# Kernel optimization log

Measured on AMD Instinct MI355X. Metric: run time of the kernel, lower is better.

## Reference

```python
import jax, jax.numpy as jnp
import numpy as np

N_WORDS, MAX_LEN, EMB, HID, VOCAB = 100000, 24, 50, 50, 200


def setup_inputs() -> dict:
    key = jax.random.key(0)
    ks = jax.random.split(key, 9)
    s = 0.1
    char_indices = jax.random.randint(ks[0], (N_WORDS, MAX_LEN), 0, VOCAB, dtype=jnp.int32)
    lengths = jax.random.randint(ks[1], (N_WORDS,), 0, MAX_LEN + 1, dtype=jnp.int32)
    emb_table = (jax.random.normal(ks[2], (VOCAB, EMB), jnp.float32) * s).at[0].set(0.0)  # padding_idx=0
    Wih_f = jax.random.normal(ks[3], (4 * HID, EMB), jnp.float32) * s
    Whh_f = jax.random.normal(ks[4], (4 * HID, HID), jnp.float32) * s
    b_f = jax.random.normal(ks[5], (4 * HID,), jnp.float32) * s  # b_ih + b_hh combined
    Wih_b = jax.random.normal(ks[6], (4 * HID, EMB), jnp.float32) * s
    Whh_b = jax.random.normal(ks[7], (4 * HID, HID), jnp.float32) * s
    b_b = jax.random.normal(ks[8], (4 * HID,), jnp.float32) * s
    return {"char_indices": char_indices, "lengths": lengths, "emb_table": emb_table,
            "Wih_f": Wih_f, "Whh_f": Whh_f, "b_f": b_f,
            "Wih_b": Wih_b, "Whh_b": Whh_b, "b_b": b_b}


def _lstm_final(emb_seq, mask_seq, Wih, Whh, b):
    # emb_seq: [T, N, E], mask_seq: [T, N] (True while t < length)
    # Masked updates freeze (h, c) past each word's length, so the final carry
    # equals PyTorch's h_n for that direction.
    hdim = Whh.shape[1]
    n = emb_seq.shape[1]

    def step(carry, xs):
        h, c = carry
        x, m = xs
        g = x @ Wih.T + h @ Whh.T + b  # [N, 4H], gate order i,f,g,o (PyTorch)
        i, f, gg, o = jnp.split(g, 4, axis=-1)
        c_new = jax.nn.sigmoid(f) * c + jax.nn.sigmoid(i) * jnp.tanh(gg)
        h_new = jax.nn.sigmoid(o) * jnp.tanh(c_new)
        m = m[:, None]
        return (jnp.where(m, h_new, h), jnp.where(m, c_new, c)), None

    h0 = jnp.zeros((n, hdim), emb_seq.dtype)
    (h_fin, _), _ = jax.lax.scan(step, (h0, h0), (emb_seq, mask_seq))
    return h_fin


def reference(char_indices, lengths, emb_table, Wih_f, Whh_f, b_f, Wih_b, Whh_b, b_b):
    n, t_max = char_indices.shape
    t = jnp.arange(t_max)
    mask = t[None, :] < lengths[:, None]  # [N, T]
    emb = emb_table[char_indices]  # [N, T, E]
    h_fwd = _lstm_final(emb.transpose(1, 0, 2), mask.T, Wih_f, Whh_f, b_f)
    # Backward direction: reverse valid prefix of each word, then scan forward.
    rev_pos = jnp.clip(lengths[:, None] - 1 - t[None, :], 0, t_max - 1)  # [N, T]
    emb_rev = emb_table[jnp.take_along_axis(char_indices, rev_pos, axis=1)]
    h_bwd = _lstm_final(emb_rev.transpose(1, 0, 2), mask.T, Wih_b, Whh_b, b_b)
    return jnp.concatenate([h_fwd, h_bwd], axis=-1)  # [N, 2H]
```

## Files before the change

kernel.cpp:

```cpp
#include <hip/hip_runtime.h>

#define EMBD 50
#define HID 50
#define BLK 256
#define NT 13
#define LOG2E 1.44269504f

typedef float f32x4 __attribute__((ext_vector_type(4)));
typedef short short8 __attribute__((ext_vector_type(8)));
typedef unsigned u32x4 __attribute__((ext_vector_type(4)));

__device__ __forceinline__ int imax(int a, int b) { return a > b ? a : b; }
__device__ __forceinline__ int imin(int a, int b) { return a < b ? a : b; }

__device__ __forceinline__ unsigned short f2bf(float f) {
    unsigned u = __float_as_uint(f);
    u += 0x7FFFu + ((u >> 16) & 1u);
    return (unsigned short)(u >> 16);
}
__device__ __forceinline__ unsigned cvtpk(float a, float b) {
    unsigned r;
    asm("v_cvt_pk_bf16_f32 %0, %1, %2" : "=v"(r) : "v"(a), "v"(b));
    return r;
}
__device__ __forceinline__ float sigm(float x) {
    return __fdividef(1.0f, 1.0f + __expf(-x));
}
__device__ __forceinline__ float tanhfast(float x) {
    float e = __expf(2.0f * x);
    return 1.0f - __fdividef(2.0f, e + 1.0f);
}

__global__ void zero_counts_kernel(int* ws) {
    if (threadIdx.x < 75) ws[threadIdx.x] = 0;
}
__global__ void hist_kernel(const int* __restrict__ lengths, int* ws, int nw) {
    __shared__ int lc[32];
    if (threadIdx.x < 32) lc[threadIdx.x] = 0;
    __syncthreads();
    int i = blockIdx.x * blockDim.x + threadIdx.x;
    if (i < nw) atomicAdd(&lc[lengths[i]], 1);
    __syncthreads();
    if (threadIdx.x < 25 && lc[threadIdx.x] > 0)
        atomicAdd(&ws[threadIdx.x], lc[threadIdx.x]);
}
__global__ void prefix_kernel(int* ws) {
    if (threadIdx.x == 0 && blockIdx.x == 0) {
        int acc = 0;
        for (int l = 0; l <= 24; ++l) { ws[25 + l] = acc; acc += ws[l]; }
    }
}
__global__ void scatter_kernel(const int* __restrict__ lengths, int* ws, int nw) {
    __shared__ int lcnt[32], lbase[32];
    if (threadIdx.x < 32) lcnt[threadIdx.x] = 0;
    __syncthreads();
    int i = blockIdx.x * blockDim.x + threadIdx.x;
    int l = 0, ticket = 0;
    bool act = i < nw;
    if (act) {
        l = lengths[i];
        ticket = atomicAdd(&lcnt[l], 1);
    }
    __syncthreads();
    if (threadIdx.x < 25 && lcnt[threadIdx.x] > 0)
        lbase[threadIdx.x] = atomicAdd(&ws[50 + threadIdx.x], lcnt[threadIdx.x]);
    __syncthreads();
    if (act) ws[100 + ws[25 + l] + lbase[l] + ticket] = i;
}

__global__ void pack_all_kernel(const float* __restrict__ emb,
                                const float* __restrict__ Wih_f, const float* __restrict__ Whh_f,
                                const float* __restrict__ b_f,
                                const float* __restrict__ Wih_b, const float* __restrict__ Whh_b,
                                const float* __restrict__ b_b,
                                unsigned short* __restrict__ xtab,
                                unsigned short* __restrict__ wp, int vocab) {
    int tid0 = blockIdx.x * blockDim.x + threadIdx.x;
    int xtTotal = 2 * vocab * NT * 16;
    if (tid0 < xtTotal) {
        int q = tid0 & 3, s = (tid0 >> 2) & 3;
        int m = (tid0 >> 4) % NT;
        int vv = (tid0 >> 4) / NT;
        int v = vv % vocab, dir = vv / vocab;
        int cnt_s = (s < 2) ? 13 : 12;
        float val = 0.0f;
        if (m < cnt_s) {
            int j = 13 * s - (s == 3 ? 1 : 0) + m;
            int row = q * HID + j;
            const float* W  = dir ? Wih_b : Wih_f;
            const float* bv = dir ? b_b   : b_f;
            float acc = bv[row];
            const float* wr = W + row * EMBD;
            const float* ev = emb + v * EMBD;
            for (int e = 0; e < EMBD; ++e) acc += wr[e] * ev[e];
            val = acc * ((q == 2) ? (2.0f * LOG2E) : LOG2E);
        }
        xtab[tid0] = f2bf(val);
        return;
    }
    int tid = tid0 - xtTotal;
    if (tid >= 2 * NT * 1024) return;
    int i    = tid & 7;
    int lane = (tid >> 3) & 63;
    int kcp  = (tid >> 9) & 1;
    int rem  = tid >> 10;
    int m    = rem % NT;
    int dir  = rem / NT;
    const float* Whh = dir ? Whh_b : Whh_f;

    int p = lane & 15, grp = lane >> 4;
    int k = (kcp + 2) * 32 + 8 * grp + i;
    int s = p >> 2, q = p & 3;
    int cnt_s = (s < 2) ? 13 : 12;
    float val = 0.0f;
    if (m < cnt_s) {
        int j = 13 * s - (s == 3 ? 1 : 0) + m;
        int row = q * HID + j;
        int kk = k - 64;
        int half = kk >> 5;
        int s2 = (kk >> 3) & 3;
        int r = kk & 7;
        int mcol = half * 8 + r;
        int cnt2 = (s2 < 2) ? 13 : 12;
        if (mcol < cnt2) {
            int jc = 13 * s2 - (s2 == 3 ? 1 : 0) + mcol;
            val = Whh[row * HID + jc] * ((q == 2) ? (2.0f * LOG2E) : LOG2E);
        }
    }
    wp[tid] = f2bf(val);
}

#define MFMA16(AW, BB, ACC) __builtin_amdgcn_mfma_f32_16x16x32_bf16((AW), (BB), (ACC), 0, 0, 0)

#define TTMH(M, XT, C, H) {                                        \
    const short8 w2 = *(const short8*)(sWl + ((M)*2+0)*512);       \
    const short8 w3 = *(const short8*)(sWl + ((M)*2+1)*512);       \
    f32x4 ah = zz;                                                 \
    ah = MFMA16(w2, bh0, ah);                                      \
    ah = MFMA16(w3, bh1, ah);                                      \
    float ai = ah[0] + __uint_as_float((XT).x << 16);              \
    float af = ah[1] + __uint_as_float((XT).x & 0xffff0000u);      \
    float ag = ah[2] + __uint_as_float((XT).y << 16);              \
    float ao = ah[3] + __uint_as_float((XT).y & 0xffff0000u);      \
    float ei = __builtin_amdgcn_exp2f(-ai);                        \
    float ef = __builtin_amdgcn_exp2f(-af);                        \
    float eg = __builtin_amdgcn_exp2f(ag);                         \
    float eo = __builtin_amdgcn_exp2f(-ao);                        \
    float a1 = 1.0f + ef, a2 = 1.0f + ei;                          \
    float a3 = eg + 1.0f, a4 = eg - 1.0f;                          \
    float p1 = a2 * a3;                                            \
    float nn = fmaf(a1, a4, (C) * p1);                             \
    float dd = a1 * p1;                                            \
    float cn = nn * __builtin_amdgcn_rcpf(dd);                     \
    float ec = __builtin_amdgcn_exp2f((2.0f * LOG2E) * cn);        \
    float b2 = ec + 1.0f, b3 = ec - 1.0f;                          \
    float qd = (1.0f + eo) * b2;                                   \
    float hn = b3 * __builtin_amdgcn_rcpf(qd);                     \
    (C) = upd ? cn : (C);                                          \
    (H) = upd ? hn : (H); }

__global__ __launch_bounds__(BLK, 2)
void bilstm_mfma_kernel(const int* __restrict__ chars,
                        const int* __restrict__ lengths,
                        const int* __restrict__ perm,
                        const unsigned short* __restrict__ xtab,
                        const unsigned short* __restrict__ wp,
                        float* __restrict__ out, int nw, int ml, int vocab)
{
    const int dir = blockIdx.y;
    __shared__ unsigned short sW[NT * 2 * 512];
    {
        const float4* src = (const float4*)(wp + dir * (NT * 2 * 512));
        float4* dst = (float4*)sW;
        for (int i = threadIdx.x; i < NT * 2 * 512 / 8; i += BLK) dst[i] = src[i];
    }
    __syncthreads();

    const int lane = threadIdx.x & 63;
    const int wv   = threadIdx.x >> 6;
    const int wcol = lane & 15;
    const int s    = lane >> 4;

    int gidx = (blockIdx.x * 4 + wv) * 16 + wcol;
    gidx = imin(gidx, nw - 1);
    gidx = nw - 1 - gidx;
    const int word = perm[gidx];
    const int len  = lengths[word];

    int lmax = len;
    lmax = imax(lmax, __shfl_xor(lmax, 1));
    lmax = imax(lmax, __shfl_xor(lmax, 2));
    lmax = imax(lmax, __shfl_xor(lmax, 4));
    lmax = imax(lmax, __shfl_xor(lmax, 8));

    const int* charp = chars + (size_t)word * ml;
    const unsigned short* sWl = sW + lane * 8;
    const unsigned short* xdir = xtab + (size_t)dir * vocab * (NT * 16) + s * 4;

    const f32x4 zz = {0.0f, 0.0f, 0.0f, 0.0f};
    float c00=0,c01=0,c02=0,c03=0,c04=0,c05=0,c06=0,c07=0,c08=0,c09=0,c10=0,c11=0,c12=0;
    float h00=0,h01=0,h02=0,h03=0,h04=0,h05=0,h06=0,h07=0,h08=0,h09=0,h10=0,h11=0,h12=0;
    short8 bh0, bh1;
#pragma unroll
    for (int i2 = 0; i2 < 8; ++i2) { bh0[i2] = 0; bh1[i2] = 0; }

    int chcur = 0;
    if (lmax > 0) {
        int pos0 = dir ? imax(len - 1, 0) : 0;
        chcur = charp[pos0];
    }

    for (int t = 0; t < lmax; ++t) {
        const unsigned short* xb = xdir + (size_t)chcur * (NT * 16);
        uint2 xt0  = *(const uint2*)(xb + 0*16);
        uint2 xt1  = *(const uint2*)(xb + 1*16);
        uint2 xt2  = *(const uint2*)(xb + 2*16);
        uint2 xt3  = *(const uint2*)(xb + 3*16);
        uint2 xt4  = *(const uint2*)(xb + 4*16);
        uint2 xt5  = *(const uint2*)(xb + 5*16);
        uint2 xt6  = *(const uint2*)(xb + 6*16);
        uint2 xt7  = *(const uint2*)(xb + 7*16);
        uint2 xt8  = *(const uint2*)(xb + 8*16);
        uint2 xt9  = *(const uint2*)(xb + 9*16);
        uint2 xt10 = *(const uint2*)(xb + 10*16);
        uint2 xt11 = *(const uint2*)(xb + 11*16);
        uint2 xt12 = *(const uint2*)(xb + 12*16);

        int tn = (t + 1 < lmax) ? t + 1 : t;
        int posn = dir ? imax(len - 1 - tn, 0) : tn;
        int chnext = charp[posn];

        const bool upd = (t < len);
        TTMH(0,  xt0,  c00, h00)
        TTMH(1,  xt1,  c01, h01)
        TTMH(2,  xt2,  c02, h02)
        TTMH(3,  xt3,  c03, h03)
        TTMH(4,  xt4,  c04, h04)
        TTMH(5,  xt5,  c05, h05)
        TTMH(6,  xt6,  c06, h06)
        TTMH(7,  xt7,  c07, h07)
        TTMH(8,  xt8,  c08, h08)
        TTMH(9,  xt9,  c09, h09)
        TTMH(10, xt10, c10, h10)
        TTMH(11, xt11, c11, h11)
        TTMH(12, xt12, c12, h12)

        u32x4 p0, p1;
        p0[0] = cvtpk(h00, h01); p0[1] = cvtpk(h02, h03);
        p0[2] = cvtpk(h04, h05); p0[3] = cvtpk(h06, h07);
        p1[0] = cvtpk(h08, h09); p1[1] = cvtpk(h10, h11);
        p1[2] = cvtpk(h12, 0.0f); p1[3] = 0u;
        bh0 = __builtin_bit_cast(short8, p0);
        bh1 = __builtin_bit_cast(short8, p1);

        chcur = chnext;
    }

    int offs = 13 * s - (s == 3 ? 1 : 0);
    float* outw = out + (size_t)word * (2 * HID) + dir * HID + offs;
    outw[0] = h00; outw[1] = h01; outw[2]  = h02; outw[3]  = h03;
    outw[4] = h04; outw[5] = h05; outw[6]  = h06; outw[7]  = h07;
    outw[8] = h08; outw[9] = h09; outw[10] = h10; outw[11] = h11;
    if (s < 2) outw[12] = h12;
}

__global__ __launch_bounds__(BLK, 2)
void bilstm_fallback_kernel(const int* __restrict__ chars,
                            const int* __restrict__ lengths,
                            const float* __restrict__ emb,
                            const float* __restrict__ Wih_f, const float* __restrict__ Whh_f, const float* __restrict__ b_f,
                            const float* __restrict__ Wih_b, const float* __restrict__ Whh_b, const float* __restrict__ b_b,
                            const int* __restrict__ perm,
                            float* __restrict__ out, int nw, int ml)
{
    const int dir = blockIdx.y;
    const float* Wih = dir ? Wih_b : Wih_f;
    const float* Whh = dir ? Whh_b : Whh_f;
    const float* bv  = dir ? b_b  : b_f;
    __shared__ float4 sWU4[HID * 100];
    __shared__ float4 sB4[HID];
    {
        float* p = (float*)sWU4;
        for (int i = threadIdx.x; i < HID * 100 * 4; i += BLK) {
            int g = i & 3, r = i >> 2, j = r / 100, k = r - j * 100;
            p[i] = (k < EMBD) ? Wih[(j + g * HID) * EMBD + k]
                              : Whh[(j + g * HID) * HID + (k - EMBD)];
        }
        if (threadIdx.x < HID) {
            int j = threadIdx.x;
            sB4[j] = make_float4(bv[j], bv[j + HID], bv[j + 2*HID], bv[j + 3*HID]);
        }
    }
    __syncthreads();
    int gid = blockIdx.x * BLK + threadIdx.x;
    if (gid >= nw) return;
    int word = perm ? perm[gid] : gid;
    int len  = lengths[word];
    float h[HID], x[EMBD], c[HID], hn[HID];
#pragma unroll
    for (int j = 0; j < HID; ++j) h[j] = 0.f;
#pragma unroll 1
    for (int j = 0; j < HID; ++j) c[j] = 0.f;
    const int* wch = chars + word * ml;
    float* op = out + (size_t)word * (2 * HID) + dir * HID;
#pragma unroll 1
    for (int t = 0; t < len; ++t) {
        int pos = dir ? (len - 1 - t) : t;
        int ch = wch[pos];
        const float2* ep = (const float2*)(emb + ch * EMBD);
#pragma unroll
        for (int k = 0; k < EMBD / 2; ++k) { float2 v = ep[k]; x[2*k] = v.x; x[2*k+1] = v.y; }
#pragma unroll 1
        for (int j = 0; j < HID; ++j) {
            const float4* wpt = sWU4 + j * 100;
            float4 bb = sB4[j];
            float gi = bb.x, gf = bb.y, gg = bb.z, go = bb.w;
#pragma unroll
            for (int k = 0; k < EMBD; ++k) {
                float4 w = wpt[k]; float xv = x[k];
                gi += w.x*xv; gf += w.y*xv; gg += w.z*xv; go += w.w*xv;
            }
#pragma unroll
            for (int k = 0; k < HID; ++k) {
                float4 w = wpt[EMBD + k]; float hv = h[k];
                gi += w.x*hv; gf += w.y*hv; gg += w.z*hv; go += w.w*hv;
            }
            float cn = sigm(gf) * c[j] + sigm(gi) * tanhfast(gg);
            c[j] = cn;
            hn[j] = sigm(go) * tanhfast(cn);
        }
#pragma unroll
        for (int j = 0; j < HID; ++j) h[j] = hn[j];
    }
#pragma unroll
    for (int j = 0; j < HID / 2; ++j)
        ((float2*)op)[j] = make_float2(h[2*j], h[2*j+1]);
}

extern "C" void kernel_launch(void* const* d_in, const int* in_sizes, int n_in,
                              void* d_out, int out_size, void* d_ws, size_t ws_size,
                              hipStream_t stream) {
    const int*   chars = (const int*)  d_in[0];
    const int*   lens  = (const int*)  d_in[1];
    const float* emb   = (const float*)d_in[2];
    const float* Wih_f = (const float*)d_in[3];
    const float* Whh_f = (const float*)d_in[4];
    const float* b_f   = (const float*)d_in[5];
    const float* Wih_b = (const float*)d_in[6];
    const float* Whh_b = (const float*)d_in[7];
    const float* b_b   = (const float*)d_in[8];
    float* out = (float*)d_out;

    const int nw    = in_sizes[1];
    const int ml    = in_sizes[0] / nw;
    const int vocab = in_sizes[2] / EMBD;

    size_t sortNeed = (size_t)(100 + nw) * 4;
    size_t xtOff    = (sortNeed + 255) & ~(size_t)255;
    size_t xtBytes  = (size_t)2 * vocab * NT * 16 * 2;
    size_t wOff     = (xtOff + xtBytes + 1023) & ~(size_t)1023;
    size_t wBytes   = (size_t)2 * NT * 1024 * 2;
    size_t need     = wOff + wBytes;

    int* ws = (int*)d_ws;
    bool haveSort = ws_size >= sortNeed;
    if (haveSort) {
        zero_counts_kernel<<<1, 128, 0, stream>>>(ws);
        hist_kernel<<<(nw + 255) / 256, 256, 0, stream>>>(lens, ws, nw);
        prefix_kernel<<<1, 1, 0, stream>>>(ws);
        scatter_kernel<<<(nw + 255) / 256, 256, 0, stream>>>(lens, ws, nw);
    }

    if (ws_size >= need && haveSort) {
        unsigned short* xtab = (unsigned short*)((char*)d_ws + xtOff);
        unsigned short* wpk  = (unsigned short*)((char*)d_ws + wOff);
        int packTot = 2 * vocab * NT * 16 + 2 * NT * 1024;
        pack_all_kernel<<<(packTot + 255) / 256, 256, 0, stream>>>(
            emb, Wih_f, Whh_f, b_f, Wih_b, Whh_b, b_b, xtab, wpk, vocab);
        dim3 grid((nw + 63) / 64, 2);
        bilstm_mfma_kernel<<<grid, BLK, 0, stream>>>(chars, lens, ws + 100, xtab, wpk,
                                                     out, nw, ml, vocab);
    } else {
        dim3 grid((nw + BLK - 1) / BLK, 2);
        bilstm_fallback_kernel<<<grid, BLK, 0, stream>>>(chars, lens, emb,
                                                         Wih_f, Whh_f, b_f,
                                                         Wih_b, Whh_b, b_b,
                                                         haveSort ? ws + 100 : nullptr,
                                                         out, nw, ml);
    }
}
```

Measured before the change: 218.4 us.

## Process two independent word groups per wavefront to interleave MFMA chains

Each wavefront now runs two independent batches of 16 words (A and B) in the same time loop. The MFMAs and gate math of the two batches are interleaved, so independent work can hide MFMA and transcendental latency in the serial recurrence, and each shared-memory weight load is reused for both batches. The grid is halved to match and launch bounds drop to one block per SIMD-pair hint, which raises register use and may reduce occupancy. Forward character positions are now clamped to the word length.

```diff
diff --git a/kernel.cpp b/kernel.cpp
--- a/kernel.cpp
+++ b/kernel.cpp
@@ -132,16 +132,11 @@
 
 #define MFMA16(AW, BB, ACC) __builtin_amdgcn_mfma_f32_16x16x32_bf16((AW), (BB), (ACC), 0, 0, 0)
 
-#define TTMH(M, XT, C, H) {                                        \
-    const short8 w2 = *(const short8*)(sWl + ((M)*2+0)*512);       \
-    const short8 w3 = *(const short8*)(sWl + ((M)*2+1)*512);       \
-    f32x4 ah = zz;                                                 \
-    ah = MFMA16(w2, bh0, ah);                                      \
-    ah = MFMA16(w3, bh1, ah);                                      \
-    float ai = ah[0] + __uint_as_float((XT).x << 16);              \
-    float af = ah[1] + __uint_as_float((XT).x & 0xffff0000u);      \
-    float ag = ah[2] + __uint_as_float((XT).y << 16);              \
-    float ao = ah[3] + __uint_as_float((XT).y & 0xffff0000u);      \
+#define GUP(AH, XT, C, H, UPD) {                                   \
+    float ai = (AH)[0] + __uint_as_float((XT).x << 16);            \
+    float af = (AH)[1] + __uint_as_float((XT).x & 0xffff0000u);    \
+    float ag = (AH)[2] + __uint_as_float((XT).y << 16);            \
+    float ao = (AH)[3] + __uint_as_float((XT).y & 0xffff0000u);    \
     float ei = __builtin_amdgcn_exp2f(-ai);                        \
     float ef = __builtin_amdgcn_exp2f(-af);                        \
     float eg = __builtin_amdgcn_exp2f(ag);                         \
@@ -156,10 +151,19 @@
     float b2 = ec + 1.0f, b3 = ec - 1.0f;                          \
     float qd = (1.0f + eo) * b2;                                   \
     float hn = b3 * __builtin_amdgcn_rcpf(qd);                     \
-    (C) = upd ? cn : (C);                                          \
-    (H) = upd ? hn : (H); }
-
-__global__ __launch_bounds__(BLK, 2)
+    (C) = (UPD) ? cn : (C);                                        \
+    (H) = (UPD) ? hn : (H); }
+
+#define TTMH2(M, XTA, XTB, CA, HA, CB, HB) {                       \
+    const short8 w2 = *(const short8*)(sWl + ((M)*2+0)*512);       \
+    const short8 w3 = *(const short8*)(sWl + ((M)*2+1)*512);       \
+    f32x4 ahA = zz, ahB = zz;                                      \
+    ahA = MFMA16(w2, bhA0, ahA);  ahB = MFMA16(w2, bhB0, ahB);     \
+    ahA = MFMA16(w3, bhA1, ahA);  ahB = MFMA16(w3, bhB1, ahB);     \
+    GUP(ahA, XTA, CA, HA, updA)                                    \
+    GUP(ahB, XTB, CB, HB, updB) }
+
+__global__ __launch_bounds__(BLK, 1)
 void bilstm_mfma_kernel(const int* __restrict__ chars,
                         const int* __restrict__ lengths,
                         const int* __restrict__ perm,
@@ -181,87 +185,111 @@
     const int wcol = lane & 15;
     const int s    = lane >> 4;
 
-    int gidx = (blockIdx.x * 4 + wv) * 16 + wcol;
-    gidx = imin(gidx, nw - 1);
-    gidx = nw - 1 - gidx;
-    const int word = perm[gidx];
-    const int len  = lengths[word];
-
-    int lmax = len;
+    int base = (blockIdx.x * 4 + wv) * 32;
+    int giA = imin(base + wcol, nw - 1);
+    int giB = imin(base + 16 + wcol, nw - 1);
+    giA = nw - 1 - giA;
+    giB = nw - 1 - giB;
+    const int wordA = perm[giA];
+    const int wordB = perm[giB];
+    const int lenA  = lengths[wordA];
+    const int lenB  = lengths[wordB];
+
+    int lmax = imax(lenA, lenB);
     lmax = imax(lmax, __shfl_xor(lmax, 1));
     lmax = imax(lmax, __shfl_xor(lmax, 2));
     lmax = imax(lmax, __shfl_xor(lmax, 4));
     lmax = imax(lmax, __shfl_xor(lmax, 8));
 
-    const int* charp = chars + (size_t)word * ml;
+    const int* charpA = chars + (size_t)wordA * ml;
+    const int* charpB = chars + (size_t)wordB * ml;
     const unsigned short* sWl = sW + lane * 8;
     const unsigned short* xdir = xtab + (size_t)dir * vocab * (NT * 16) + s * 4;
 
     const f32x4 zz = {0.0f, 0.0f, 0.0f, 0.0f};
-    float c00=0,c01=0,c02=0,c03=0,c04=0,c05=0,c06=0,c07=0,c08=0,c09=0,c10=0,c11=0,c12=0;
-    float h00=0,h01=0,h02=0,h03=0,h04=0,h05=0,h06=0,h07=0,h08=0,h09=0,h10=0,h11=0,h12=0;
-    short8 bh0, bh1;
-#pragma unroll
-    for (int i2 = 0; i2 < 8; ++i2) { bh0[i2] = 0; bh1[i2] = 0; }
-
-    int chcur = 0;
+    float cA00=0,cA01=0,cA02=0,cA03=0,cA04=0,cA05=0,cA06=0,cA07=0,cA08=0,cA09=0,cA10=0,cA11=0,cA12=0;
+    float hA00=0,hA01=0,hA02=0,hA03=0,hA04=0,hA05=0,hA06=0,hA07=0,hA08=0,hA09=0,hA10=0,hA11=0,hA12=0;
+    float cB00=0,cB01=0,cB02=0,cB03=0,cB04=0,cB05=0,cB06=0,cB07=0,cB08=0,cB09=0,cB10=0,cB11=0,cB12=0;
+    float hB00=0,hB01=0,hB02=0,hB03=0,hB04=0,hB05=0,hB06=0,hB07=0,hB08=0,hB09=0,hB10=0,hB11=0,hB12=0;
+    short8 bhA0, bhA1, bhB0, bhB1;
+#pragma unroll
+    for (int i2 = 0; i2 < 8; ++i2) { bhA0[i2]=0; bhA1[i2]=0; bhB0[i2]=0; bhB1[i2]=0; }
+
+    int chA = 0, chB = 0;
     if (lmax > 0) {
-        int pos0 = dir ? imax(len - 1, 0) : 0;
-        chcur = charp[pos0];
+        int pA = dir ? imax(lenA - 1, 0) : 0;
+        int pB = dir ? imax(lenB - 1, 0) : 0;
+        chA = charpA[pA];
+        chB = charpB[pB];
     }
 
     for (int t = 0; t < lmax; ++t) {
-        const unsigned short* xb = xdir + (size_t)chcur * (NT * 16);
-        uint2 xt0  = *(const uint2*)(xb + 0*16);
-        uint2 xt1  = *(const uint2*)(xb + 1*16);
-        uint2 xt2  = *(const uint2*)(xb + 2*16);
-        uint2 xt3  = *(const uint2*)(xb + 3*16);
-        uint2 xt4  = *(const uint2*)(xb + 4*16);
-        uint2 xt5  = *(const uint2*)(xb + 5*16);
-        uint2 xt6  = *(const uint2*)(xb + 6*16);
-        uint2 xt7  = *(const uint2*)(xb + 7*16);
-        uint2 xt8  = *(const uint2*)(xb + 8*16);
-        uint2 xt9  = *(const uint2*)(xb + 9*16);
-        uint2 xt10 = *(const uint2*)(xb + 10*16);
-        uint2 xt11 = *(const uint2*)(xb + 11*16);
-        uint2 xt12 = *(const uint2*)(xb + 12*16);
+        const unsigned short* xa = xdir + (size_t)chA * (NT * 16);
+        const unsigned short* xb = xdir + (size_t)chB * (NT * 16);
+        uint2 xtA0  = *(const uint2*)(xa + 0*16);  uint2 xtB0  = *(const uint2*)(xb + 0*16);
+        uint2 xtA1  = *(const uint2*)(xa + 1*16);  uint2 xtB1  = *(const uint2*)(xb + 1*16);
+        uint2 xtA2  = *(const uint2*)(xa + 2*16);  uint2 xtB2  = *(const uint2*)(xb + 2*16);
+        uint2 xtA3  = *(const uint2*)(xa + 3*16);  uint2 xtB3  = *(const uint2*)(xb + 3*16);
+        uint2 xtA4  = *(const uint2*)(xa + 4*16);  uint2 xtB4  = *(const uint2*)(xb + 4*16);
+        uint2 xtA5  = *(const uint2*)(xa + 5*16);  uint2 xtB5  = *(const uint2*)(xb + 5*16);
+        uint2 xtA6  = *(const uint2*)(xa + 6*16);  uint2 xtB6  = *(const uint2*)(xb + 6*16);
+        uint2 xtA7  = *(const uint2*)(xa + 7*16);  uint2 xtB7  = *(const uint2*)(xb + 7*16);
+        uint2 xtA8  = *(const uint2*)(xa + 8*16);  uint2 xtB8  = *(const uint2*)(xb + 8*16);
+        uint2 xtA9  = *(const uint2*)(xa + 9*16);  uint2 xtB9  = *(const uint2*)(xb + 9*16);
+        uint2 xtA10 = *(const uint2*)(xa + 10*16); uint2 xtB10 = *(const uint2*)(xb + 10*16);
+        uint2 xtA11 = *(const uint2*)(xa + 11*16); uint2 xtB11 = *(const uint2*)(xb + 11*16);
+        uint2 xtA12 = *(const uint2*)(xa + 12*16); uint2 xtB12 = *(const uint2*)(xb + 12*16);
 
         int tn = (t + 1 < lmax) ? t + 1 : t;
-        int posn = dir ? imax(len - 1 - tn, 0) : tn;
-        int chnext = charp[posn];
-
-        const bool upd = (t < len);
-        TTMH(0,  xt0,  c00, h00)
-        TTMH(1,  xt1,  c01, h01)
-        TTMH(2,  xt2,  c02, h02)
-        TTMH(3,  xt3,  c03, h03)
-        TTMH(4,  xt4,  c04, h04)
-        TTMH(5,  xt5,  c05, h05)
-        TTMH(6,  xt6,  c06, h06)
-        TTMH(7,  xt7,  c07, h07)
-        TTMH(8,  xt8,  c08, h08)
-        TTMH(9,  xt9,  c09, h09)
-        TTMH(10, xt10, c10, h10)
-        TTMH(11, xt11, c11, h11)
-        TTMH(12, xt12, c12, h12)
+        int pAn = dir ? imax(lenA - 1 - tn, 0) : imin(tn, imax(lenA - 1, 0));
+        int pBn = dir ? imax(lenB - 1 - tn, 0) : imin(tn, imax(lenB - 1, 0));
+        int chAn = charpA[pAn];
+        int chBn = charpB[pBn];
+
+        const bool updA = (t < lenA);
+        const bool updB = (t < lenB);
+        TTMH2(0,  xtA0,  xtB0,  cA00, hA00, cB00, hB00)
+        TTMH2(1,  xtA1,  xtB1,  cA01, hA01, cB01, hB01)
+        TTMH2(2,  xtA2,  xtB2,  cA02, hA02, cB02, hB02)
+        TTMH2(3,  xtA3,  xtB3,  cA03, hA03, cB03, hB03)
+        TTMH2(4,  xtA4,  xtB4,  cA04, hA04, cB04, hB04)
+        TTMH2(5,  xtA5,  xtB5,  cA05, hA05, cB05, hB05)
+        TTMH2(6,  xtA6,  xtB6,  cA06, hA06, cB06, hB06)
+        TTMH2(7,  xtA7,  xtB7,  cA07, hA07, cB07, hB07)
+        TTMH2(8,  xtA8,  xtB8,  cA08, hA08, cB08, hB08)
+        TTMH2(9,  xtA9,  xtB9,  cA09, hA09, cB09, hB09)
+        TTMH2(10, xtA10, xtB10, cA10, hA10, cB10, hB10)
+        TTMH2(11, xtA11, xtB11, cA11, hA11, cB11, hB11)
+        TTMH2(12, xtA12, xtB12, cA12, hA12, cB12, hB12)
 
         u32x4 p0, p1;
-        p0[0] = cvtpk(h00, h01); p0[1] = cvtpk(h02, h03);
-        p0[2] = cvtpk(h04, h05); p0[3] = cvtpk(h06, h07);
-        p1[0] = cvtpk(h08, h09); p1[1] = cvtpk(h10, h11);
-        p1[2] = cvtpk(h12, 0.0f); p1[3] = 0u;
-        bh0 = __builtin_bit_cast(short8, p0);
-        bh1 = __builtin_bit_cast(short8, p1);
-
-        chcur = chnext;
+        p0[0] = cvtpk(hA00, hA01); p0[1] = cvtpk(hA02, hA03);
+        p0[2] = cvtpk(hA04, hA05); p0[3] = cvtpk(hA06, hA07);
+        p1[0] = cvtpk(hA08, hA09); p1[1] = cvtpk(hA10, hA11);
+        p1[2] = cvtpk(hA12, 0.0f); p1[3] = 0u;
+        bhA0 = __builtin_bit_cast(short8, p0);
+        bhA1 = __builtin_bit_cast(short8, p1);
+        p0[0] = cvtpk(hB00, hB01); p0[1] = cvtpk(hB02, hB03);
+        p0[2] = cvtpk(hB04, hB05); p0[3] = cvtpk(hB06, hB07);
+        p1[0] = cvtpk(hB08, hB09); p1[1] = cvtpk(hB10, hB11);
+        p1[2] = cvtpk(hB12, 0.0f); p1[3] = 0u;
+        bhB0 = __builtin_bit_cast(short8, p0);
+        bhB1 = __builtin_bit_cast(short8, p1);
+
+        chA = chAn; chB = chBn;
     }
 
     int offs = 13 * s - (s == 3 ? 1 : 0);
-    float* outw = out + (size_t)word * (2 * HID) + dir * HID + offs;
-    outw[0] = h00; outw[1] = h01; outw[2]  = h02; outw[3]  = h03;
-    outw[4] = h04; outw[5] = h05; outw[6]  = h06; outw[7]  = h07;
-    outw[8] = h08; outw[9] = h09; outw[10] = h10; outw[11] = h11;
-    if (s < 2) outw[12] = h12;
+    float* oA = out + (size_t)wordA * (2 * HID) + dir * HID + offs;
+    oA[0] = hA00; oA[1] = hA01; oA[2]  = hA02; oA[3]  = hA03;
+    oA[4] = hA04; oA[5] = hA05; oA[6]  = hA06; oA[7]  = hA07;
+    oA[8] = hA08; oA[9] = hA09; oA[10] = hA10; oA[11] = hA11;
+    if (s < 2) oA[12] = hA12;
+    float* oB = out + (size_t)wordB * (2 * HID) + dir * HID + offs;
+    oB[0] = hB00; oB[1] = hB01; oB[2]  = hB02; oB[3]  = hB03;
+    oB[4] = hB04; oB[5] = hB05; oB[6]  = hB06; oB[7]  = hB07;
+    oB[8] = hB08; oB[9] = hB09; oB[10] = hB10; oB[11] = hB11;
+    if (s < 2) oB[12] = hB12;
 }
 
 __global__ __launch_bounds__(BLK, 2)
@@ -377,7 +405,7 @@
         int packTot = 2 * vocab * NT * 16 + 2 * NT * 1024;
         pack_all_kernel<<<(packTot + 255) / 256, 256, 0, stream>>>(
             emb, Wih_f, Whh_f, b_f, Wih_b, Whh_b, b_b, xtab, wpk, vocab);
-        dim3 grid((nw + 63) / 64, 2);
+        dim3 grid((nw + 127) / 128, 2);
         bilstm_mfma_kernel<<<grid, BLK, 0, stream>>>(chars, lens, ws + 100, xtab, wpk,
                                                      out, nw, ml, vocab);
     } else {
```

Result: slower. 255.5 us (+17.0%).
